# Kernel tuning notes

Hardware: AMD Instinct MI355X
Metric: run time of the kernel (lower is better)

The kernel has to match this reference:

```python
import jax, jax.numpy as jnp
import numpy as np
import math

HAD_BLOCK = 1024


def fwht(x):
    """Fast Walsh-Hadamard transform along the last axis (size must be power of 2)."""
    orig_shape = x.shape
    n = orig_shape[-1]
    x = x.reshape(-1, n)
    h = 1
    while h < n:  # log2(n) stages; static Python loop, jit-friendly
        x = x.reshape(-1, n // (2 * h), 2, h)
        a = x[:, :, 0, :]
        b = x[:, :, 1, :]
        x = jnp.stack([a + b, a - b], axis=2).reshape(-1, n)
        h *= 2
    return x.reshape(orig_shape)


def setup_inputs() -> dict:
    key = jax.random.key(0)
    kx, kw = jax.random.split(key)
    B, S, D_in, D_out = 4, 4096, 4096, 4096
    x = jax.random.normal(kx, (B, S, D_in), dtype=jnp.float32)
    # nn.Parameter(weight / sqrt(had_block_size)) in __init__
    weight = jax.random.normal(kw, (D_out, D_in), dtype=jnp.float32) / math.sqrt(HAD_BLOCK)
    return {"x": x, "weight": weight}


def reference(x, weight):
    n = x.shape[-1]
    padded = ((n - 1) // HAD_BLOCK + 1) * HAD_BLOCK
    if padded != n:
        pad_width = [(0, 0)] * (x.ndim - 1) + [(0, padded - n)]
        x = jnp.pad(x, pad_width)
    mult = padded // HAD_BLOCK
    xb = x.reshape(x.shape[:-1] + (mult, HAD_BLOCK))
    xb = fwht(xb) * (1.0 / math.sqrt(HAD_BLOCK))
    xh = xb.reshape(x.shape[:-1] + (mult * HAD_BLOCK,))
    # F.linear: x @ weight.T
    return jnp.einsum('bsi,oi->bso', xh, weight)
```

## Files before the change

kernel.cpp:

```cpp
#include <hip/hip_runtime.h>
#include <hip/hip_bf16.h>
#include <stdint.h>


typedef __attribute__((ext_vector_type(8))) short    short8;
typedef __attribute__((ext_vector_type(4))) float    f32x4;
typedef __attribute__((ext_vector_type(8))) uint16_t u16x8;

static constexpr int MDIM = 16384;
static constexpr int NDIM = 4096;
static constexpr int KDIM = 4096;
static constexpr int BM = 256, BN = 256, BK = 64;
static constexpr int NT = KDIM / BK;

__device__ __forceinline__ uint16_t f2bf(float f) {
  union { float f; uint32_t u; } c; c.f = f;
  uint32_t u = c.u;
  return (uint16_t)((u + 0x7FFFu + ((u >> 16) & 1u)) >> 16);
}

__global__ __launch_bounds__(256) void cvt_x_kernel(const float* __restrict__ x,
                                                    uint16_t* __restrict__ xb, int n8) {
  int stride = gridDim.x * blockDim.x;
  for (int t = blockIdx.x * blockDim.x + threadIdx.x; t < n8; t += stride) {
    const float4* p = reinterpret_cast<const float4*>(x + (size_t)t * 8);
    float4 a = p[0], b = p[1];
    u16x8 o;
    o[0] = f2bf(a.x); o[1] = f2bf(a.y); o[2] = f2bf(a.z); o[3] = f2bf(a.w);
    o[4] = f2bf(b.x); o[5] = f2bf(b.y); o[6] = f2bf(b.z); o[7] = f2bf(b.w);
    *reinterpret_cast<u16x8*>(xb + (size_t)t * 8) = o;
  }
}

__global__ __launch_bounds__(256) void fwht_w_kernel(const float* __restrict__ W,
                                                     uint16_t* __restrict__ Wh) {
  __shared__ float s[1024];
  const int tid = threadIdx.x;
  const size_t base = (size_t)blockIdx.x * 1024;
  reinterpret_cast<float4*>(s)[tid] = reinterpret_cast<const float4*>(W + base)[tid];
  __syncthreads();
  for (int h = 1; h < 1024; h <<= 1) {
    #pragma unroll
    for (int pp = 0; pp < 2; ++pp) {
      int p = tid + pp * 256;
      int q = p & (h - 1);
      int i = ((p - q) << 1) | q;
      float a = s[i], b = s[i + h];
      s[i] = a + b;
      s[i + h] = a - b;
    }
    __syncthreads();
  }
  #pragma unroll
  for (int pp = 0; pp < 4; ++pp) {
    int i = tid + pp * 256;
    Wh[base + i] = f2bf(s[i] * 0.03125f);
  }
}


#define FENCE asm volatile("" ::: "memory")
#define SBAR  do { FENCE; __builtin_amdgcn_s_barrier(); \
                   __builtin_amdgcn_sched_barrier(0); } while (0)
#define LGKM0 do { asm volatile("s_waitcnt lgkmcnt(0)" ::: "memory"); \
                   __builtin_amdgcn_sched_barrier(0); } while (0)
#define VMC(n) asm volatile("s_waitcnt vmcnt(" #n ")" ::: "memory")

#define LDA4(DST, BUF, MLO, KOFF)                                              \
  do { _Pragma("unroll")                                                       \
    for (int m_ = 0; m_ < 4; ++m_)                                             \
      DST[m_] = *(const short8*)(aRd + (BUF)*32768 + ((MLO)+m_)*2048 + (KOFF)); \
  } while (0)

#define LDB4(DST, BUF, KOFF)                                                   \
  do { _Pragma("unroll")                                                       \
    for (int n_ = 0; n_ < 4; ++n_)                                             \
      DST[n_] = *(const short8*)(bRd + (BUF)*32768 + n_*2048 + (KOFF));        \
  } while (0)

#define MF16(AF, BF, MB)                                                       \
  do { __builtin_amdgcn_s_setprio(1);                                          \
    _Pragma("unroll")                                                          \
    for (int m_ = 0; m_ < 4; ++m_)                                             \
      _Pragma("unroll")                                                        \
      for (int n_ = 0; n_ < 4; ++n_)                                           \
        acc[(MB)+m_][n_] = __builtin_amdgcn_mfma_f32_16x16x32_bf16(            \
            AF[m_], BF[n_], acc[(MB)+m_][n_], 0, 0, 0);                        \
    __builtin_amdgcn_s_setprio(0);                                             \
  } while (0)

#define ITER(T1, T2, T3, FIN)                                                  \
  do {                                                                         \
    short8 aL[4], aH[4], bK[4];                                                \
     stageA(1, 0, (T1));                                              \
    LDA4(aL, 0, 0, k0off); LDB4(bK, 0, k0off);                                 \
    SBAR; LGKM0; MF16(aL, bK, 0); SBAR;                                        \
     stageA(1, 1, (T1)); stageB(1, 1, (T1));                          \
    LDA4(aH, 0, 4, k0off);                                                     \
    SBAR; LGKM0; MF16(aH, bK, 4); SBAR;                                        \
     LDA4(aL, 0, 0, k1off); LDB4(bK, 0, k1off);                       \
    SBAR; LGKM0; MF16(aL, bK, 0); SBAR;                                        \
     if (!(FIN)) stageB(0, 0, (T2));                                  \
    LDA4(aH, 0, 4, k1off);                                                     \
    if (FIN) { VMC(0); } else { VMC(2); }                                      \
    SBAR; LGKM0; MF16(aH, bK, 4); SBAR;                                        \
     if (!(FIN)) stageA(0, 0, (T2));                                  \
    LDA4(aL, 1, 0, k0off); LDB4(bK, 1, k0off);                                 \
    SBAR; LGKM0; MF16(aL, bK, 0); SBAR;                                        \
     if (!(FIN)) { stageA(0, 1, (T2)); stageB(0, 1, (T2)); }          \
    LDA4(aH, 1, 4, k0off);                                                     \
    SBAR; LGKM0; MF16(aH, bK, 4); SBAR;                                        \
     LDA4(aL, 1, 0, k1off); LDB4(bK, 1, k1off);                       \
    SBAR; LGKM0; MF16(aL, bK, 0); SBAR;                                        \
     if (!(FIN)) { stageB(1, 0, (T3)); }                              \
    LDA4(aH, 1, 4, k1off);                                                     \
    if (!(FIN)) { VMC(2); }                                                    \
    SBAR; LGKM0; MF16(aH, bK, 4); SBAR;                                        \
  } while (0)

__global__ __launch_bounds__(512, 2) void gemm_bt(const uint16_t* __restrict__ A,
                                                  const uint16_t* __restrict__ B,
                                                  float* __restrict__ C) {
  __shared__ __align__(16) uint16_t Ab[2][BM * BK];
  __shared__ __align__(16) uint16_t Bb[2][BN * BK];

  const int tid = threadIdx.x;
  const int wv  = tid >> 6;
  const int l   = tid & 63;

  const int wg = ((blockIdx.x & 7) << 7) | (blockIdx.x >> 3);
  const int tm = wg >> 4;
  const int tn = wg & 15;
  const int wm = wv >> 2;
  const int wn = wv & 3;

  const int t8  = tid >> 3;
  const int swz = (tid & 7) ^ ((tid >> 4) & 7);
  const uint16_t* sA = A + (size_t)(tm * BM + t8) * KDIM + swz * 8;
  const uint16_t* sB = B + (size_t)(tn * BN + t8) * KDIM + swz * 8;

  auto stageA = [&](int buf, int half, int tk) {
    #pragma unroll
    for (int j = 0; j < 2; ++j)
      __builtin_amdgcn_global_load_lds(
          (const __attribute__((address_space(1))) unsigned int*)
              (sA + (size_t)(half * 128 + j * 64) * KDIM + tk * BK),
          (__attribute__((address_space(3))) unsigned int*)
              ((char*)&Ab[buf][0] + half * 16384 + j * 8192 + wv * 1024),
          16, 0, 0);
  };
  auto stageB = [&](int buf, int half, int tk) {
    #pragma unroll
    for (int j = 0; j < 2; ++j)
      __builtin_amdgcn_global_load_lds(
          (const __attribute__((address_space(1))) unsigned int*)
              (sB + (size_t)(half * 128 + j * 64) * KDIM + tk * BK),
          (__attribute__((address_space(3))) unsigned int*)
              ((char*)&Bb[buf][0] + half * 16384 + j * 8192 + wv * 1024),
          16, 0, 0);
  };

  const int lA = l & 15, hi = l >> 4;
  const int xr = (lA >> 1) & 7;
  const int k0off = (hi ^ xr) * 16;
  const int k1off = k0off ^ 64;
  const char* aRd = (const char*)&Ab[0][0] + (wm * 128 + lA) * 128;
  const char* bRd = (const char*)&Bb[0][0] + (wn * 64 + lA) * 128;

  f32x4 acc[8][4] = {};

  stageA(0, 0, 0); stageA(0, 1, 0); stageB(0, 0, 0); stageB(0, 1, 0);
  stageB(1, 0, 1);
  VMC(2);
  SBAR;

  #pragma unroll 1
  for (int i = 0; i < NT / 2 - 1; ++i)
    ITER(2 * i + 1, 2 * i + 2, 2 * i + 3, 0);
  ITER(NT - 1, 0, 0, 1);

  float* Cp = C + (size_t)(tm * BM + wm * 128) * NDIM + tn * BN + wn * 64;
  const int co = hi * 4;
  #pragma unroll
  for (int m = 0; m < 8; ++m)
    #pragma unroll
    for (int n = 0; n < 4; ++n)
      #pragma unroll
      for (int j = 0; j < 4; ++j)
        Cp[(size_t)(m * 16 + co + j) * NDIM + n * 16 + lA] = acc[m][n][j];
}

extern "C" void kernel_launch(void* const* d_in, const int* in_sizes, int n_in,
                              void* d_out, int out_size, void* d_ws, size_t ws_size,
                              hipStream_t stream) {
  (void)in_sizes; (void)n_in; (void)out_size; (void)ws_size;
  const float* x = (const float*)d_in[0];
  const float* w = (const float*)d_in[1];
  float* out = (float*)d_out;

  uint16_t* xb = (uint16_t*)d_ws;
  uint16_t* wh = xb + (size_t)MDIM * KDIM;

  cvt_x_kernel<<<2048, 256, 0, stream>>>(x, xb, (int)((MDIM * (size_t)KDIM) / 8));
  fwht_w_kernel<<<(NDIM * KDIM) / 1024, 256, 0, stream>>>(w, wh);
  gemm_bt<<<(MDIM / BM) * (NDIM / BN), 512, 0, stream>>>(xb, wh, out);
}
```

Measured before the change: 694.1 us.

## Halve barriers per GEMM sub-step and interleave global staging after LDS reads

Restructures the GEMM main loop so each MFMA sub-step uses one workgroup barrier instead of two. LDS fragment reads are now issued before the global-to-LDS staging loads, and the vmcnt waits are placed after the MFMA blocks. VMC gains a sched_barrier so the compiler cannot move instructions across the wait. The goal is to cut barrier stalls and overlap global loads with LDS reads and MFMA work, at the cost of tighter and less obvious hazard ordering on the double-buffered LDS.

```diff
diff --git a/kernel.cpp b/kernel.cpp
--- a/kernel.cpp
+++ b/kernel.cpp
@@ -64,7 +64,8 @@
                    __builtin_amdgcn_sched_barrier(0); } while (0)
 #define LGKM0 do { asm volatile("s_waitcnt lgkmcnt(0)" ::: "memory"); \
                    __builtin_amdgcn_sched_barrier(0); } while (0)
-#define VMC(n) asm volatile("s_waitcnt vmcnt(" #n ")" ::: "memory")
+#define VMC(n) do { asm volatile("s_waitcnt vmcnt(" #n ")" ::: "memory"); \
+                    __builtin_amdgcn_sched_barrier(0); } while (0)
 
 #define LDA4(DST, BUF, MLO, KOFF)                                              \
   do { _Pragma("unroll")                                                       \
@@ -92,30 +93,38 @@
 #define ITER(T1, T2, T3, FIN)                                                  \
   do {                                                                         \
     short8 aL[4], aH[4], bK[4];                                                \
-     stageA(1, 0, (T1));                                              \
-    LDA4(aL, 0, 0, k0off); LDB4(bK, 0, k0off);                                 \
-    SBAR; LGKM0; MF16(aL, bK, 0); SBAR;                                        \
-     stageA(1, 1, (T1)); stageB(1, 1, (T1));                          \
+     SBAR;                                                            \
+    LDB4(bK, 0, k0off); LDA4(aL, 0, 0, k0off);                                 \
+    stageA(1, 0, (T1));                                                        \
+    LGKM0; MF16(aL, bK, 0);                                                    \
+     SBAR;                                                            \
     LDA4(aH, 0, 4, k0off);                                                     \
-    SBAR; LGKM0; MF16(aH, bK, 4); SBAR;                                        \
-     LDA4(aL, 0, 0, k1off); LDB4(bK, 0, k1off);                       \
-    SBAR; LGKM0; MF16(aL, bK, 0); SBAR;                                        \
-     if (!(FIN)) stageB(0, 0, (T2));                                  \
+    stageA(1, 1, (T1)); stageB(1, 1, (T1));                                    \
+    LGKM0; MF16(aH, bK, 4);                                                    \
+     SBAR;                                                            \
+    LDB4(bK, 0, k1off); LDA4(aL, 0, 0, k1off);                                 \
+    LGKM0; MF16(aL, bK, 0);                                                    \
+     SBAR;                                                            \
     LDA4(aH, 0, 4, k1off);                                                     \
+    if (!(FIN)) stageB(0, 0, (T2));                                            \
+    LGKM0; MF16(aH, bK, 4);                                                    \
     if (FIN) { VMC(0); } else { VMC(2); }                                      \
-    SBAR; LGKM0; MF16(aH, bK, 4); SBAR;                                        \
-     if (!(FIN)) stageA(0, 0, (T2));                                  \
-    LDA4(aL, 1, 0, k0off); LDB4(bK, 1, k0off);                                 \
-    SBAR; LGKM0; MF16(aL, bK, 0); SBAR;                                        \
-     if (!(FIN)) { stageA(0, 1, (T2)); stageB(0, 1, (T2)); }          \
+     SBAR;                                                            \
+    LDB4(bK, 1, k0off); LDA4(aL, 1, 0, k0off);                                 \
+    if (!(FIN)) stageA(0, 0, (T2));                                            \
+    LGKM0; MF16(aL, bK, 0);                                                    \
+     SBAR;                                                            \
     LDA4(aH, 1, 4, k0off);                                                     \
-    SBAR; LGKM0; MF16(aH, bK, 4); SBAR;                                        \
-     LDA4(aL, 1, 0, k1off); LDB4(bK, 1, k1off);                       \
-    SBAR; LGKM0; MF16(aL, bK, 0); SBAR;                                        \
-     if (!(FIN)) { stageB(1, 0, (T3)); }                              \
+    if (!(FIN)) { stageA(0, 1, (T2)); stageB(0, 1, (T2)); }                    \
+    LGKM0; MF16(aH, bK, 4);                                                    \
+     SBAR;                                                            \
+    LDB4(bK, 1, k1off); LDA4(aL, 1, 0, k1off);                                 \
+    LGKM0; MF16(aL, bK, 0);                                                    \
+     SBAR;                                                            \
     LDA4(aH, 1, 4, k1off);                                                     \
+    if (!(FIN)) stageB(1, 0, (T3));                                            \
+    LGKM0; MF16(aH, bK, 4);                                                    \
     if (!(FIN)) { VMC(2); }                                                    \
-    SBAR; LGKM0; MF16(aH, bK, 4); SBAR;                                        \
   } while (0)
 
 __global__ __launch_bounds__(512, 2) void gemm_bt(const uint16_t* __restrict__ A,
@@ -172,7 +181,6 @@
   stageA(0, 0, 0); stageA(0, 1, 0); stageB(0, 0, 0); stageB(0, 1, 0);
   stageB(1, 0, 1);
   VMC(2);
-  SBAR;
 
   #pragma unroll 1
   for (int i = 0; i < NT / 2 - 1; ++i)
```

After: 596.4 us. 14.1% less time.
